# Optimization experiments

Hardware: AMD Instinct MI355X
Metric: run time of the kernel (lower is better)

Reference implementation:

```python
import jax, jax.numpy as jnp
import numpy as np

B, D, M = 16384, 512, 16

def setup_inputs() -> dict:
    key = jax.random.key(0)
    k1, k2, k3 = jax.random.split(key, 3)
    z = jax.random.normal(k1, (B, D), dtype=jnp.float32)
    # Psi: n_dynamics small [D,D] operators (orthogonal-init in torch; random here)
    Psi = jax.random.normal(k2, (M, D, D), dtype=jnp.float32) * 0.001
    gate_tokens = jax.random.normal(k3, (M, D), dtype=jnp.float32) * (1.0 / np.sqrt(D))
    t = jnp.zeros((1,), dtype=jnp.float32)  # unused by forward, kept for signature parity
    return {"t": t, "z": z, "Psi": Psi, "gate_tokens": gate_tokens}

def reference(t, z, Psi, gate_tokens):
    # scores[b,m,e] = (z @ Psi_m)[b,e]  -- batched small GEMM over M dynamics
    scores = jnp.einsum('bd,mde->bme', z, Psi)
    # gate logits and sparse-soft gates: relu(2*sigmoid(logits) - 1)
    logits = jnp.einsum('bme,me->bm', scores, gate_tokens)
    gates = jax.nn.relu(2.0 * jax.nn.sigmoid(logits) - 1.0)
    # dz[b,e] = sum_m gates[b,m] * scores[b,m,e]
    dz = jnp.einsum('bm,bme->be', gates, scores)
    return dz
```

## Files before the change

kernel.cpp:

```cpp
#include <hip/hip_runtime.h>
#include <hip/hip_bf16.h>

#define B_N 16384
#define D_N 512
#define M_N 16

typedef __attribute__((ext_vector_type(4))) float  f32x4;
typedef __attribute__((ext_vector_type(8))) short  s16x8;

__device__ __forceinline__ short bf16_of(float f) {
  union { float f; unsigned u; } v; v.f = f;
  unsigned r = v.u + 0x7fffu + ((v.u >> 16) & 1u);
  return (short)(r >> 16);
}
__device__ __forceinline__ float f32_of_bf16(unsigned short u) {
  union { unsigned u; float f; } v; v.u = ((unsigned)u) << 16; return v.f;
}
__device__ __forceinline__ void gload_lds16(const void* g, void* l) {
  __builtin_amdgcn_global_load_lds(
      (const __attribute__((address_space(1))) unsigned*)g,
      (__attribute__((address_space(3))) unsigned*)l, 16, 0, 0);
}

#define MFMA_ACC(d, x, y) d = __builtin_amdgcn_mfma_f32_16x16x32_bf16(x, y, d, 0, 0, 0)

__global__ void k_trw(const float* __restrict__ Psi, const float* __restrict__ gt,
                      short* __restrict__ Psib, float* __restrict__ wT) {
  int m = blockIdx.y, d0 = blockIdx.x << 6;
  __shared__ float tile[64][65];
  __shared__ float gs[D_N];
  int t = threadIdx.x;
  for (int i = t; i < D_N; i += 256) gs[i] = gt[m * D_N + i];
  int r = t >> 2, q = t & 3;
  float wacc = 0.f;
  const float* src = Psi + (size_t)m * D_N * D_N;
  short* dst = Psib + (size_t)m * D_N * D_N;
  for (int e0 = 0; e0 < D_N; e0 += 64) {
    __syncthreads();
    #pragma unroll
    for (int j = 0; j < 4; ++j) {
      int idx = t + (j << 8);
      int rr = idx >> 4, c4 = idx & 15;
      *(f32x4*)&tile[rr][c4 * 4] = *(const f32x4*)(src + (size_t)(d0 + rr) * D_N + e0 + c4 * 4);
    }
    __syncthreads();
    #pragma unroll
    for (int k = 0; k < 16; ++k) wacc += tile[r][q * 16 + k] * gs[e0 + q * 16 + k];
    #pragma unroll
    for (int it = 0; it < 2; ++it) {
      int idx = t + (it << 8);
      int el = idx >> 3, jb = idx & 7;
      int e = e0 + el;
      s16x8 o;
      #pragma unroll
      for (int k = 0; k < 8; ++k) o[k] = bf16_of(tile[jb * 8 + k][el]);
      int db = jb ^ (e & 7);
      *(s16x8*)(dst + (size_t)e * D_N + d0 + db * 8) = o;
    }
  }
  wacc += __shfl_xor(wacc, 1);
  wacc += __shfl_xor(wacc, 2);
  if (q == 0) wT[(d0 + r) * M_N + m] = wacc;
}

__global__ void k_gz(const float* __restrict__ z, const float* __restrict__ wT,
                     short* __restrict__ zb, unsigned short* __restrict__ gatesb) {
  __shared__ float zs[16][D_N];
  int t = threadIdx.x;
  size_t b0 = (size_t)blockIdx.x * 16;
  #pragma unroll
  for (int j = 0; j < 8; ++j) {
    int idx = t + (j << 8);
    int r = idx >> 7, c4 = idx & 127;
    *(f32x4*)&zs[r][c4 * 4] = *(const f32x4*)(z + (b0 + r) * D_N + c4 * 4);
  }
  __syncthreads();
  int r = t >> 4, m = t & 15;
  float s0 = 0.f, s1 = 0.f, s2 = 0.f, s3 = 0.f;
  #pragma unroll 4
  for (int e = 0; e < D_N; e += 4) {
    s0 += zs[r][e + 0] * wT[(e + 0) * M_N + m];
    s1 += zs[r][e + 1] * wT[(e + 1) * M_N + m];
    s2 += zs[r][e + 2] * wT[(e + 2) * M_N + m];
    s3 += zs[r][e + 3] * wT[(e + 3) * M_N + m];
  }
  float s = (s0 + s1) + (s2 + s3);
  float sig = 1.f / (1.f + expf(-s));
  gatesb[(b0 + r) * M_N + m] = (unsigned short)bf16_of(fmaxf(2.f * sig - 1.f, 0.f));
  #pragma unroll
  for (int j = 0; j < 4; ++j) {
    int idx = t + (j << 8);
    int rr = idx >> 6, blk = idx & 63;
    int chunk = blk >> 3, ib = blk & 7;
    int sb = ib ^ (rr & 7);
    const float* sp = &zs[rr][chunk * 64 + sb * 8];
    s16x8 o;
    #pragma unroll
    for (int k = 0; k < 8; ++k) o[k] = bf16_of(sp[k]);
    *(s16x8*)(zb + (b0 + rr) * D_N + blk * 8) = o;
  }
}

__global__ __launch_bounds__(512, 2) void k_gemm(
    const char* __restrict__ zb, const unsigned short* __restrict__ gatesb,
    const char* __restrict__ pb, float* __restrict__ dz) {
  __shared__ __align__(128) char smem[139264];

  const int tid = threadIdx.x;
  const int lane = tid & 63;
  const int wid = tid >> 6;
  const int wr = wid >> 1;
  const int wc = wid & 1;
  const int bid = blockIdx.x;
  const int xcd = bid & 7;
  const int g8 = bid >> 3;
  const int bcol = g8 & 3;
  const int brow = xcd * 8 + (g8 >> 2);

  {
    s16x8 gv = *(const s16x8*)(gatesb + ((size_t)brow << 12) + ((size_t)tid << 3));
    unsigned short* gl = (unsigned short*)(smem + 131072);
    int row = tid >> 1, mbase = (tid & 1) << 3;
    #pragma unroll
    for (int k = 0; k < 8; ++k)
      gl[(mbase + k) * 256 + row] = (unsigned short)gv[k];
  }

  const int rsub = lane >> 3, cbyte = (lane & 7) << 4;

  auto stageA = [&](int ab, int dc) {
    #pragma unroll
    for (int j = 0; j < 4; ++j) {
      const char* g = zb + (((size_t)(brow * 256 + wid * 8 + j * 64 + rsub)) << 10)
                      + (dc << 7) + cbyte;
      gload_lds16(g, smem + ab * 32768 + (wid << 10) + (j << 13));
    }
  };
  auto stageB = [&](int s) {
    int m = s & 15, dc = s >> 4, q = s & 3;
    #pragma unroll
    for (int j = 0; j < 2; ++j) {
      const char* g = pb + (((size_t)(m * 512 + bcol * 128 + wid * 8 + j * 64 + rsub)) << 10)
                      + (dc << 7) + cbyte;
      gload_lds16(g, smem + 65536 + q * 16384 + (wid << 10) + (j << 13));
    }
  };

  const int lrow = lane & 15;
  const int swz = (lrow & 7) << 4;
  const int kq16 = (((lane >> 4) << 4)) ^ swz;
  const int offY = ((wr * 64 + lrow) << 7) + kq16;
  const int offX = ((wc * 64 + lrow) << 7) + kq16;

  f32x4 acc[4][4] = {};
  f32x4 accm[4][4] = {};
  s16x8 areg[4][2];
  s16x8 bx[4], by[4];

  stageA(0, 0);
  stageB(0); stageB(1); stageB(2);
  asm volatile("s_waitcnt vmcnt(0) lgkmcnt(0)" ::: "memory");
  __builtin_amdgcn_s_barrier();
  #pragma unroll
  for (int i = 0; i < 4; ++i)
    bx[i] = *(const s16x8*)(smem + 65536 + (offX + i * 2048));

  for (int s = 0; s < 128; ++s) {
    const int m = s & 15, dc = s >> 4;
    const char* bbase_cur = smem + 65536 + (s & 3) * 16384;
    const char* bbase_nxt = smem + 65536 + ((s + 1) & 3) * 16384;

    if (m == 0) {
      const char* abase = smem + (dc & 1) * 32768;
      #pragma unroll
      for (int j = 0; j < 4; ++j) {
        areg[j][0] = *(const s16x8*)(abase + (offY + j * 2048));
        areg[j][1] = *(const s16x8*)(abase + ((offY + j * 2048) ^ 64));
      }
    }
    #pragma unroll
    for (int i = 0; i < 4; ++i)
      by[i] = *(const s16x8*)(bbase_cur + ((offX + i * 2048) ^ 64));
    if (s + 3 < 128) stageB(s + 3);
    if (m == 11 && dc < 7) stageA((dc & 1) ^ 1, dc + 1);
    float gj[4];
    {
      const unsigned short* gl = (const unsigned short*)(smem + 131072);
      #pragma unroll
      for (int j = 0; j < 4; ++j)
        gj[j] = f32_of_bf16(gl[m * 256 + wr * 64 + j * 16 + lrow]);
    }
    __builtin_amdgcn_s_setprio(1);
    #pragma unroll
    for (int i = 0; i < 4; ++i)
      #pragma unroll
      for (int j = 0; j < 4; ++j)
        MFMA_ACC(accm[i][j], bx[i], areg[j][0]);
    __builtin_amdgcn_s_setprio(0);

    if (s < 127) {
      #pragma unroll
      for (int i = 0; i < 4; ++i)
        bx[i] = *(const s16x8*)(bbase_nxt + (offX + i * 2048));
    }
    __builtin_amdgcn_s_setprio(1);
    #pragma unroll
    for (int i = 0; i < 4; ++i)
      #pragma unroll
      for (int j = 0; j < 4; ++j)
        MFMA_ACC(accm[i][j], by[i], areg[j][1]);
    __builtin_amdgcn_s_setprio(0);
    #pragma unroll
    for (int i = 0; i < 4; ++i)
      #pragma unroll
      for (int j = 0; j < 4; ++j) {
        #pragma unroll
        for (int jj = 0; jj < 4; ++jj)
          acc[i][j][jj] += gj[j] * accm[i][j][jj];
        accm[i][j] = f32x4{0.f, 0.f, 0.f, 0.f};
      }

    if (dc < 7 && (m == 11 || m == 12))
      asm volatile("s_waitcnt vmcnt(6)" ::: "memory");
    else if (s >= 125)
      asm volatile("s_waitcnt vmcnt(0)" ::: "memory");
    else
      asm volatile("s_waitcnt vmcnt(2)" ::: "memory");
    __builtin_amdgcn_s_barrier();
  }

  #pragma unroll
  for (int i = 0; i < 4; ++i) {
    int e = bcol * 128 + wc * 64 + i * 16 + ((lane >> 4) << 2);
    #pragma unroll
    for (int j = 0; j < 4; ++j) {
      size_t b = (size_t)brow * 256 + wr * 64 + j * 16 + lrow;
      *(f32x4*)(dz + b * D_N + e) = acc[i][j];
    }
  }
}

extern "C" void kernel_launch(void* const* d_in, const int* in_sizes, int n_in,
                              void* d_out, int out_size, void* d_ws, size_t ws_size,
                              hipStream_t stream) {
  const float* z   = (const float*)d_in[1];
  const float* Psi = (const float*)d_in[2];
  const float* gt  = (const float*)d_in[3];
  float* dz = (float*)d_out;

  float* wT = (float*)d_ws;
  unsigned short* gatesb = (unsigned short*)((char*)d_ws + 32768);
  short* Psib = (short*)((char*)d_ws + 32768 + 524288);
  short* zb16 = Psib + (size_t)M_N * D_N * D_N;

  k_trw <<<dim3(8, M_N), dim3(256), 0, stream>>>(Psi, gt, Psib, wT);
  k_gz  <<<dim3(B_N / 16), dim3(256), 0, stream>>>(z, wT, zb16, gatesb);
  k_gemm<<<dim3(256), dim3(512), 0, stream>>>((const char*)zb16, gatesb,
                                              (const char*)Psib, dz);
}
```

Baseline: 157.6 us.

## Halve GEMM row tile, double-buffer B, raise occupancy to four blocks

```diff
diff --git a/kernel.cpp b/kernel.cpp
--- a/kernel.cpp
+++ b/kernel.cpp
@@ -6,7 +6,9 @@
 #define M_N 16
 
 typedef __attribute__((ext_vector_type(4))) float  f32x4;
+typedef __attribute__((ext_vector_type(2))) float  f32x2;
 typedef __attribute__((ext_vector_type(8))) short  s16x8;
+typedef __attribute__((ext_vector_type(4))) unsigned short u16x4;
 
 __device__ __forceinline__ short bf16_of(float f) {
   union { float f; unsigned u; } v; v.f = f;
@@ -23,6 +25,7 @@
 }
 
 #define MFMA_ACC(d, x, y) d = __builtin_amdgcn_mfma_f32_16x16x32_bf16(x, y, d, 0, 0, 0)
+#define MFMA_Z(d, x, y)   d = __builtin_amdgcn_mfma_f32_16x16x32_bf16(x, y, FZERO, 0, 0, 0)
 
 __global__ void k_trw(const float* __restrict__ Psi, const float* __restrict__ gt,
                       short* __restrict__ Psib, float* __restrict__ wT) {
@@ -101,10 +104,11 @@
   }
 }
 
-__global__ __launch_bounds__(512, 2) void k_gemm(
+__global__ __launch_bounds__(512, 4) void k_gemm(
     const char* __restrict__ zb, const unsigned short* __restrict__ gatesb,
     const char* __restrict__ pb, float* __restrict__ dz) {
-  __shared__ __align__(128) char smem[139264];
+  __shared__ __align__(128) char smem[73728];
+  float* glf = (float*)(smem + 65536);
 
   const int tid = threadIdx.x;
   const int lane = tid & 63;
@@ -115,117 +119,106 @@
   const int xcd = bid & 7;
   const int g8 = bid >> 3;
   const int bcol = g8 & 3;
-  const int brow = xcd * 8 + (g8 >> 2);
+  const int brow = xcd * 16 + (g8 >> 2);
 
   {
-    s16x8 gv = *(const s16x8*)(gatesb + ((size_t)brow << 12) + ((size_t)tid << 3));
-    unsigned short* gl = (unsigned short*)(smem + 131072);
-    int row = tid >> 1, mbase = (tid & 1) << 3;
-    #pragma unroll
-    for (int k = 0; k < 8; ++k)
-      gl[(mbase + k) * 256 + row] = (unsigned short)gv[k];
+    int row = tid >> 2, g4 = tid & 3;
+    u16x4 gv = *(const u16x4*)(gatesb + ((size_t)(brow * 128 + row) << 4) + (g4 << 2));
+    #pragma unroll
+    for (int k = 0; k < 4; ++k)
+      glf[(g4 * 4 + k) * 128 + row] = f32_of_bf16(gv[k]);
   }
 
   const int rsub = lane >> 3, cbyte = (lane & 7) << 4;
 
   auto stageA = [&](int ab, int dc) {
     #pragma unroll
-    for (int j = 0; j < 4; ++j) {
-      const char* g = zb + (((size_t)(brow * 256 + wid * 8 + j * 64 + rsub)) << 10)
+    for (int j = 0; j < 2; ++j) {
+      const char* g = zb + (((size_t)(brow * 128 + wid * 8 + j * 64 + rsub)) << 10)
                       + (dc << 7) + cbyte;
-      gload_lds16(g, smem + ab * 32768 + (wid << 10) + (j << 13));
+      gload_lds16(g, smem + ab * 16384 + (wid << 10) + (j << 13));
     }
   };
-  auto stageB = [&](int s) {
-    int m = s & 15, dc = s >> 4, q = s & 3;
+  auto stageB = [&](int m, int dc, int qb) {
     #pragma unroll
     for (int j = 0; j < 2; ++j) {
       const char* g = pb + (((size_t)(m * 512 + bcol * 128 + wid * 8 + j * 64 + rsub)) << 10)
                       + (dc << 7) + cbyte;
-      gload_lds16(g, smem + 65536 + q * 16384 + (wid << 10) + (j << 13));
+      gload_lds16(g, smem + 32768 + qb * 16384 + (wid << 10) + (j << 13));
     }
   };
 
   const int lrow = lane & 15;
-  const int swz = (lrow & 7) << 4;
-  const int kq16 = (((lane >> 4) << 4)) ^ swz;
-  const int offY = ((wr * 64 + lrow) << 7) + kq16;
+  const int kq16 = (((lane >> 4) << 4)) ^ ((lrow & 7) << 4);
+  const int offY = ((wr * 32 + lrow) << 7) + kq16;
   const int offX = ((wc * 64 + lrow) << 7) + kq16;
-
-  f32x4 acc[4][4] = {};
-  f32x4 accm[4][4] = {};
-  s16x8 areg[4][2];
-  s16x8 bx[4], by[4];
+  const int grow = wr * 32 + lrow;
+
+  f32x4 acc[4][2] = {};
+  f32x4 accm[4][2];
+  s16x8 areg[2][2];
+  const f32x4 FZERO = {0.f, 0.f, 0.f, 0.f};
 
   stageA(0, 0);
-  stageB(0); stageB(1); stageB(2);
+  stageB(0, 0, 0);
   asm volatile("s_waitcnt vmcnt(0) lgkmcnt(0)" ::: "memory");
   __builtin_amdgcn_s_barrier();
-  #pragma unroll
-  for (int i = 0; i < 4; ++i)
-    bx[i] = *(const s16x8*)(smem + 65536 + (offX + i * 2048));
-
+
+  #pragma unroll 1
   for (int s = 0; s < 128; ++s) {
     const int m = s & 15, dc = s >> 4;
-    const char* bbase_cur = smem + 65536 + (s & 3) * 16384;
-    const char* bbase_nxt = smem + 65536 + ((s + 1) & 3) * 16384;
+
+    if (s < 127) stageB((s + 1) & 15, (s + 1) >> 4, (s + 1) & 1);
+    if (m == 14 && dc < 7) stageA((dc & 1) ^ 1, dc + 1);
 
     if (m == 0) {
-      const char* abase = smem + (dc & 1) * 32768;
+      const char* abase = smem + (dc & 1) * 16384;
       #pragma unroll
-      for (int j = 0; j < 4; ++j) {
+      for (int j = 0; j < 2; ++j) {
         areg[j][0] = *(const s16x8*)(abase + (offY + j * 2048));
         areg[j][1] = *(const s16x8*)(abase + ((offY + j * 2048) ^ 64));
       }
     }
-    #pragma unroll
-    for (int i = 0; i < 4; ++i)
-      by[i] = *(const s16x8*)(bbase_cur + ((offX + i * 2048) ^ 64));
-    if (s + 3 < 128) stageB(s + 3);
-    if (m == 11 && dc < 7) stageA((dc & 1) ^ 1, dc + 1);
-    float gj[4];
+    float g0 = glf[m * 128 + grow];
+    float g1 = glf[m * 128 + grow + 16];
+
+    const char* bbase = smem + 32768 + (s & 1) * 16384;
     {
-      const unsigned short* gl = (const unsigned short*)(smem + 131072);
-      #pragma unroll
-      for (int j = 0; j < 4; ++j)
-        gj[j] = f32_of_bf16(gl[m * 256 + wr * 64 + j * 16 + lrow]);
-    }
-    __builtin_amdgcn_s_setprio(1);
-    #pragma unroll
-    for (int i = 0; i < 4; ++i)
-      #pragma unroll
-      for (int j = 0; j < 4; ++j)
-        MFMA_ACC(accm[i][j], bx[i], areg[j][0]);
-    __builtin_amdgcn_s_setprio(0);
-
-    if (s < 127) {
-      #pragma unroll
-      for (int i = 0; i < 4; ++i)
-        bx[i] = *(const s16x8*)(bbase_nxt + (offX + i * 2048));
-    }
-    __builtin_amdgcn_s_setprio(1);
-    #pragma unroll
-    for (int i = 0; i < 4; ++i)
-      #pragma unroll
-      for (int j = 0; j < 4; ++j)
-        MFMA_ACC(accm[i][j], by[i], areg[j][1]);
-    __builtin_amdgcn_s_setprio(0);
-    #pragma unroll
-    for (int i = 0; i < 4; ++i)
-      #pragma unroll
-      for (int j = 0; j < 4; ++j) {
-        #pragma unroll
-        for (int jj = 0; jj < 4; ++jj)
-          acc[i][j][jj] += gj[j] * accm[i][j][jj];
-        accm[i][j] = f32x4{0.f, 0.f, 0.f, 0.f};
-      }
-
-    if (dc < 7 && (m == 11 || m == 12))
-      asm volatile("s_waitcnt vmcnt(6)" ::: "memory");
-    else if (s >= 125)
-      asm volatile("s_waitcnt vmcnt(0)" ::: "memory");
-    else
-      asm volatile("s_waitcnt vmcnt(2)" ::: "memory");
+      s16x8 b0 = *(const s16x8*)(bbase + (offX));
+      s16x8 b1 = *(const s16x8*)(bbase + (offX + 2048));
+      s16x8 b2 = *(const s16x8*)(bbase + (offX + 4096));
+      s16x8 b3 = *(const s16x8*)(bbase + (offX + 6144));
+      __builtin_amdgcn_s_setprio(1);
+      MFMA_Z(accm[0][0], b0, areg[0][0]); MFMA_Z(accm[0][1], b0, areg[1][0]);
+      MFMA_Z(accm[1][0], b1, areg[0][0]); MFMA_Z(accm[1][1], b1, areg[1][0]);
+      MFMA_Z(accm[2][0], b2, areg[0][0]); MFMA_Z(accm[2][1], b2, areg[1][0]);
+      MFMA_Z(accm[3][0], b3, areg[0][0]); MFMA_Z(accm[3][1], b3, areg[1][0]);
+      __builtin_amdgcn_s_setprio(0);
+    }
+    {
+      s16x8 b0 = *(const s16x8*)(bbase + (offX ^ 64));
+      s16x8 b1 = *(const s16x8*)(bbase + ((offX + 2048) ^ 64));
+      s16x8 b2 = *(const s16x8*)(bbase + ((offX + 4096) ^ 64));
+      s16x8 b3 = *(const s16x8*)(bbase + ((offX + 6144) ^ 64));
+      __builtin_amdgcn_s_setprio(1);
+      MFMA_ACC(accm[0][0], b0, areg[0][1]); MFMA_ACC(accm[0][1], b0, areg[1][1]);
+      MFMA_ACC(accm[1][0], b1, areg[0][1]); MFMA_ACC(accm[1][1], b1, areg[1][1]);
+      MFMA_ACC(accm[2][0], b2, areg[0][1]); MFMA_ACC(accm[2][1], b2, areg[1][1]);
+      MFMA_ACC(accm[3][0], b3, areg[0][1]); MFMA_ACC(accm[3][1], b3, areg[1][1]);
+      __builtin_amdgcn_s_setprio(0);
+    }
+    #pragma unroll
+    for (int i = 0; i < 4; ++i) {
+      f32x2 ga = {g0, g0}, gb = {g1, g1};
+      f32x2* a0 = (f32x2*)&acc[i][0];
+      f32x2* a1 = (f32x2*)&acc[i][1];
+      const f32x2* m0p = (const f32x2*)&accm[i][0];
+      const f32x2* m1p = (const f32x2*)&accm[i][1];
+      a0[0] += ga * m0p[0]; a0[1] += ga * m0p[1];
+      a1[0] += gb * m1p[0]; a1[1] += gb * m1p[1];
+    }
+
+    asm volatile("s_waitcnt vmcnt(0)" ::: "memory");
     __builtin_amdgcn_s_barrier();
   }
 
@@ -233,8 +226,8 @@
   for (int i = 0; i < 4; ++i) {
     int e = bcol * 128 + wc * 64 + i * 16 + ((lane >> 4) << 2);
     #pragma unroll
-    for (int j = 0; j < 4; ++j) {
-      size_t b = (size_t)brow * 256 + wr * 64 + j * 16 + lrow;
+    for (int j = 0; j < 2; ++j) {
+      size_t b = (size_t)brow * 128 + wr * 32 + j * 16 + lrow;
       *(f32x4*)(dz + b * D_N + e) = acc[i][j];
     }
   }
@@ -255,6 +248,6 @@
 
   k_trw <<<dim3(8, M_N), dim3(256), 0, stream>>>(Psi, gt, Psib, wT);
   k_gz  <<<dim3(B_N / 16), dim3(256), 0, stream>>>(z, wT, zb16, gatesb);
-  k_gemm<<<dim3(256), dim3(512), 0, stream>>>((const char*)zb16, gatesb,
+  k_gemm<<<dim3(512), dim3(512), 0, stream>>>((const char*)zb16, gatesb,
                                               (const char*)Psib, dz);
 }
```

Result: slower. 161.3 us (+2.4%).
